# Performance work log

Measured on AMD Instinct MI355X. Metric: run time of the kernel, lower is better.

The kernel has to match this reference:

```python
import jax, jax.numpy as jnp
import numpy as np

EPS = 1e-5
DOWNSAMPLE = 0.5


def setup_inputs() -> dict:
    key = jax.random.key(0)
    k1, k2, k3 = jax.random.split(key, 3)
    B, C, H, W = 32, 256, 128, 128
    x = jax.random.normal(k1, (B, C, H, W), dtype=jnp.float32)
    # 1x1 conv: weight [3, C], bias [3]
    conv_w = jax.random.normal(k2, (3, C), dtype=jnp.float32) / np.sqrt(C).astype(np.float32)
    conv_b = jax.random.normal(k3, (3,), dtype=jnp.float32) * 0.01
    return {"x": x, "conv_w": conv_w, "conv_b": conv_b}


def reference(x, conv_w, conv_b):
    B, C, H, W = x.shape
    dh = int(round(H * DOWNSAMPLE))
    dw = int(round(W * DOWNSAMPLE))

    # 1x1 conv producing 3 channels: 2 offset + 1 attention logit
    oa = jnp.einsum('bchw,oc->bohw', x, conv_w) + conv_b[None, :, None, None]
    offset = oa[:, :2]                      # [B,2,H,W]
    attention = jnp.exp(oa[:, 2:3])         # [B,1,H,W]

    # normalized destination coordinates = base grid + offset, clamped
    gy = jnp.broadcast_to((jnp.arange(H, dtype=x.dtype) / H)[:, None], (H, W))
    gx = jnp.broadcast_to((jnp.arange(W, dtype=x.dtype) / W)[None, :], (H, W))
    base = jnp.stack([gy, gx])              # [2,H,W]
    dest = jnp.clip(base[None] + offset, 0.0, 1.0 - EPS)
    dy = jnp.floor(dest[:, 0] * dh)
    dx = jnp.floor(dest[:, 1] * dw)
    cell = (dy * dw + dx).astype(jnp.int32)  # [B,H,W] spatial cell index

    # full flat destination index over (batch, channel, cell)
    b_off = jnp.arange(B, dtype=jnp.int32)[:, None, None, None] * (C * dh * dw)
    c_off = jnp.arange(C, dtype=jnp.int32)[None, :, None, None] * (dh * dw)
    destination = cell[:, None] + b_off + c_off  # [B,C,H,W]

    # scatter-add attention-weighted features
    xw = (x * attention).reshape(-1)
    feat = jax.ops.segment_sum(xw, destination.reshape(-1), num_segments=B * C * dh * dw)

    # scatter-add attention per (batch, cell) for normalization
    a_idx = cell + jnp.arange(B, dtype=jnp.int32)[:, None, None] * (dh * dw)
    att_sum = jax.ops.segment_sum(attention.reshape(-1), a_idx.reshape(-1), num_segments=B * dh * dw) + EPS

    out = feat.reshape(B, C, dh, dw) / att_sum.reshape(B, 1, dh, dw)
    return (out, offset, destination)
```

## Files before the change

kernel.cpp:

```cpp
#include <hip/hip_runtime.h>
#include <math.h>

#define NB 32
#define NC 256
#define NH 128
#define NW 128
#define NDH 64
#define NDW 64
#define NHW (NH * NW)
#define NCELLS (NDH * NDW)
#define OUT0_N (NB * NC * NCELLS)
#define OUT1_BASE OUT0_N
#define OUT1_N (NB * 2 * NHW)
#define OUT2_BASE (OUT1_BASE + OUT1_N)

#define EPSF 1e-5f

typedef unsigned short u16;
typedef unsigned int   u32;

#define WS_CELLS   ((size_t)0)
#define WS_ATTS    (WS_CELLS + (size_t)NB*NHW*2)
#define WS_ECOMB   (WS_ATTS + (size_t)NB*NHW*4)
#define WS_ASUM    (WS_ECOMB + (size_t)NB*NHW*4)

__device__ __forceinline__ u16 f32_to_bf16_rn(float f) {
    const u32 u = __float_as_uint(f);
    return (u16)((u + 0x7FFFu + ((u >> 16) & 1u)) >> 16);
}

__global__ __launch_bounds__(256) void k_cells(
    const float* __restrict__ x, const float* __restrict__ cw,
    const float* __restrict__ cb, float* __restrict__ out,
    u16* __restrict__ cells, float* __restrict__ atts)
{
    __shared__ float cwS[3][NC];
    __shared__ float red[256][13];

    const int t    = threadIdx.x;
    const int blk  = blockIdx.x;
    const int b    = blk >> 8;
    const int tile = blk & 255;
    const int h    = tile >> 1;
    const int w0   = (tile & 1) << 6;
    const int pixbase = h * NW + w0;

    cwS[0][t] = cw[t];
    cwS[1][t] = cw[NC + t];
    cwS[2][t] = cw[2 * NC + t];
    __syncthreads();

    const int ct = t >> 4;
    const int pg = (t & 15) << 2;
    const float* xb = x + (size_t)b * NC * NHW + pixbase + pg;

    float p00 = 0, p01 = 0, p02 = 0;
    float p10 = 0, p11 = 0, p12 = 0;
    float p20 = 0, p21 = 0, p22 = 0;
    float p30 = 0, p31 = 0, p32 = 0;

    #pragma unroll
    for (int i = 0; i < 16; ++i) {
        const int c = (i << 4) + ct;
        const float4 xv = *reinterpret_cast<const float4*>(xb + (size_t)c * NHW);
        const float wc0 = cwS[0][c], wc1 = cwS[1][c], wc2 = cwS[2][c];
        p00 += xv.x * wc0; p01 += xv.x * wc1; p02 += xv.x * wc2;
        p10 += xv.y * wc0; p11 += xv.y * wc1; p12 += xv.y * wc2;
        p20 += xv.z * wc0; p21 += xv.z * wc1; p22 += xv.z * wc2;
        p30 += xv.w * wc0; p31 += xv.w * wc1; p32 += xv.w * wc2;
    }

    red[t][0]  = p00; red[t][1]  = p01; red[t][2]  = p02;
    red[t][3]  = p10; red[t][4]  = p11; red[t][5]  = p12;
    red[t][6]  = p20; red[t][7]  = p21; red[t][8]  = p22;
    red[t][9]  = p30; red[t][10] = p31; red[t][11] = p32;
    __syncthreads();

    if (t < 64) {
        const int px   = t;
        const int row0 = px >> 2;
        const int col  = (px & 3) * 3;
        float s0 = 0, s1 = 0, s2 = 0;
        #pragma unroll
        for (int j = 0; j < 16; ++j) {
            const int r = row0 + (j << 4);
            s0 += red[r][col];
            s1 += red[r][col + 1];
            s2 += red[r][col + 2];
        }
        const float off0 = s0 + cb[0];
        const float off1 = s1 + cb[1];
        const float att  = expf(s2 + cb[2]);

        const float gy = (float)h * (1.0f / NH);
        const float gx = (float)(w0 + px) * (1.0f / NW);
        const float dyf = fminf(fmaxf(gy + off0, 0.0f), 0.99999f);
        const float dxf = fminf(fmaxf(gx + off1, 0.0f), 0.99999f);
        const int dy = (int)floorf(dyf * (float)NDH);
        const int dx = (int)floorf(dxf * (float)NDW);
        const int cell = dy * NDW + dx;

        cells[b * NHW + pixbase + px] = (u16)cell;
        atts [b * NHW + pixbase + px] = att;

        const int o1 = OUT1_BASE + b * 2 * NHW + pixbase + px;
        out[o1]       = off0;
        out[o1 + NHW] = off1;
    }
}

__global__ __launch_bounds__(1024) void k_sort(
    const u16* __restrict__ cells, const float* __restrict__ atts,
    u32* __restrict__ ecomb, float* __restrict__ asum)
{
    __shared__ u32   hist[NCELLS];
    __shared__ float as_[NCELLS];
    __shared__ u32   ts[1024];

    const int t = threadIdx.x;
    const int b = blockIdx.x;
    const u16*   cb_ = cells + b * NHW;
    const float* ab_ = atts + b * NHW;

    #pragma unroll
    for (int j = 0; j < 4; ++j) { hist[t + 1024 * j] = 0u; as_[t + 1024 * j] = 0.f; }
    __syncthreads();

    #pragma unroll
    for (int j = 0; j < 16; ++j) {
        const int p  = t + 1024 * j;
        const int cl = cb_[p];
        atomicAdd(&hist[cl], 1u);
        atomicAdd(&as_[cl], ab_[p]);
    }
    __syncthreads();

    const u32 h0 = hist[4 * t], h1 = hist[4 * t + 1], h2 = hist[4 * t + 2], h3 = hist[4 * t + 3];
    const u32 T  = h0 + h1 + h2 + h3;
    ts[t] = T;
    __syncthreads();
    for (int off = 1; off < 1024; off <<= 1) {
        const u32 v = (t >= off) ? ts[t - off] : 0u;
        __syncthreads();
        ts[t] += v;
        __syncthreads();
    }
    const u32 base = ts[t] - T;
    hist[4 * t]     = base;
    hist[4 * t + 1] = base + h0;
    hist[4 * t + 2] = base + h0 + h1;
    hist[4 * t + 3] = base + h0 + h1 + h2;

    #pragma unroll
    for (int j = 0; j < 4; ++j)
        asum[b * NCELLS + t + 1024 * j] = as_[t + 1024 * j];
    __syncthreads();

    #pragma unroll
    for (int j = 0; j < 16; ++j) {
        const int p  = t + 1024 * j;
        const int cl = cb_[p];
        const u32 pos = atomicAdd(&hist[cl], 1u);
        ecomb[b * NHW + pos] = ((u32)cl << 16) | (u32)p;
    }
}

#define BF16V(E) __uint_as_float((u32)xpl[(E) & 0xFFFFu] << 16)
#define ACCUM(CUR, S, E, V)                                                   \
    {                                                                         \
        const int cl_ = (int)((E) >> 16);                                     \
        if (cl_ != (CUR)) { atomicAdd(&acc[(CUR)], (S)); (S) = 0.f; (CUR) = cl_; } \
        (S) += (V);                                                           \
    }

__global__ __launch_bounds__(256) void k_gdest(
    const float* __restrict__ x, const float* __restrict__ atts,
    const u16* __restrict__ cells, const u32* __restrict__ ecomb,
    const float* __restrict__ asum, float* __restrict__ out)
{
    __shared__ u16   xpl[NHW];
    __shared__ float acc[NCELLS];

    const int t   = threadIdx.x;
    const int blk = blockIdx.x;
    const int b   = blk >> 8;
    const int c   = blk & 255;

    const float4* xp4  = reinterpret_cast<const float4*>(x + (size_t)(b * NC + c) * NHW);
    const float4* at4  = reinterpret_cast<const float4*>(atts + b * NHW);
    float4*       acc4 = reinterpret_cast<float4*>(acc);

    #pragma unroll
    for (int k = 0; k < 16; ++k) {
        const int idx = t + 256 * k;
        const float4 xv = xp4[idx];
        const float4 av = at4[idx];
        const u32 lo = (u32)f32_to_bf16_rn(xv.x * av.x)
                     | ((u32)f32_to_bf16_rn(xv.y * av.y) << 16);
        const u32 hi = (u32)f32_to_bf16_rn(xv.z * av.z)
                     | ((u32)f32_to_bf16_rn(xv.w * av.w) << 16);
        *reinterpret_cast<uint2*>(&xpl[idx * 4]) = make_uint2(lo, hi);
    }
    const float4 z4 = make_float4(0.f, 0.f, 0.f, 0.f);
    #pragma unroll
    for (int k = 0; k < 4; ++k) acc4[t + 256 * k] = z4;

    {
        const uint2* cl2 = reinterpret_cast<const uint2*>(cells + b * NHW);
        float4* dst4 = reinterpret_cast<float4*>(out + OUT2_BASE + (size_t)(b * NC + c) * NHW);
        const int basec = (b * NC + c) * NCELLS;
        #pragma unroll
        for (int k = 0; k < 16; ++k) {
            const int idx = t + 256 * k;
            const uint2 cc = cl2[idx];
            float4 dv;
            dv.x = (float)(basec + (int)(cc.x & 0xFFFFu));
            dv.y = (float)(basec + (int)(cc.x >> 16));
            dv.z = (float)(basec + (int)(cc.y & 0xFFFFu));
            dv.w = (float)(basec + (int)(cc.y >> 16));
            dst4[idx] = dv;
        }
    }
    __syncthreads();

    {
        const u32* el = ecomb + b * NHW + t * 64;
        float s0 = 0.f, s1 = 0.f, s2 = 0.f, s3 = 0.f;
        int   c0 = (int)(el[0]  >> 16);
        int   c1 = (int)(el[16] >> 16);
        int   c2 = (int)(el[32] >> 16);
        int   c3 = (int)(el[48] >> 16);

        #pragma unroll
        for (int ch = 0; ch < 4; ++ch) {
            const uint4 e0 = *reinterpret_cast<const uint4*>(el + ch * 4);
            const uint4 e1 = *reinterpret_cast<const uint4*>(el + 16 + ch * 4);
            const uint4 e2 = *reinterpret_cast<const uint4*>(el + 32 + ch * 4);
            const uint4 e3 = *reinterpret_cast<const uint4*>(el + 48 + ch * 4);
            const float v00 = BF16V(e0.x), v01 = BF16V(e0.y), v02 = BF16V(e0.z), v03 = BF16V(e0.w);
            const float v10 = BF16V(e1.x), v11 = BF16V(e1.y), v12 = BF16V(e1.z), v13 = BF16V(e1.w);
            const float v20 = BF16V(e2.x), v21 = BF16V(e2.y), v22 = BF16V(e2.z), v23 = BF16V(e2.w);
            const float v30 = BF16V(e3.x), v31 = BF16V(e3.y), v32 = BF16V(e3.z), v33 = BF16V(e3.w);
            ACCUM(c0, s0, e0.x, v00); ACCUM(c1, s1, e1.x, v10); ACCUM(c2, s2, e2.x, v20); ACCUM(c3, s3, e3.x, v30);
            ACCUM(c0, s0, e0.y, v01); ACCUM(c1, s1, e1.y, v11); ACCUM(c2, s2, e2.y, v21); ACCUM(c3, s3, e3.y, v31);
            ACCUM(c0, s0, e0.z, v02); ACCUM(c1, s1, e1.z, v12); ACCUM(c2, s2, e2.z, v22); ACCUM(c3, s3, e3.z, v32);
            ACCUM(c0, s0, e0.w, v03); ACCUM(c1, s1, e1.w, v13); ACCUM(c2, s2, e2.w, v23); ACCUM(c3, s3, e3.w, v33);
        }
        atomicAdd(&acc[c0], s0);
        atomicAdd(&acc[c1], s1);
        atomicAdd(&acc[c2], s2);
        atomicAdd(&acc[c3], s3);
    }
    __syncthreads();

    const float4* as4 = reinterpret_cast<const float4*>(asum + b * NCELLS);
    float4* ob4 = reinterpret_cast<float4*>(out + (size_t)(b * NC + c) * NCELLS);
    #pragma unroll
    for (int k = 0; k < 4; ++k) {
        float4 a = acc4[t + 256 * k];
        const float4 sv = as4[t + 256 * k];
        a.x /= (sv.x + EPSF);
        a.y /= (sv.y + EPSF);
        a.z /= (sv.z + EPSF);
        a.w /= (sv.w + EPSF);
        ob4[t + 256 * k] = a;
    }
}

extern "C" void kernel_launch(void* const* d_in, const int* in_sizes, int n_in,
                              void* d_out, int out_size, void* d_ws, size_t ws_size,
                              hipStream_t stream)
{
    (void)in_sizes; (void)n_in; (void)out_size; (void)ws_size;
    const float* x  = (const float*)d_in[0];
    const float* cw = (const float*)d_in[1];
    const float* cb = (const float*)d_in[2];
    float* out = (float*)d_out;
    char*  ws  = (char*)d_ws;

    u16*   cells = (u16*)  (ws + WS_CELLS);
    float* atts  = (float*)(ws + WS_ATTS);
    u32*   ecomb = (u32*)  (ws + WS_ECOMB);
    float* asum  = (float*)(ws + WS_ASUM);

    k_cells<<<dim3(NB * 256), dim3(256),  0, stream>>>(x, cw, cb, out, cells, atts);
    k_sort <<<dim3(NB),       dim3(1024), 0, stream>>>(cells, atts, ecomb, asum);
    k_gdest<<<dim3(NB * NC),  dim3(256),  0, stream>>>(x, atts, cells, ecomb, asum, out);
}
```

Measured before the change: 476.7 us.

## Move destination output into conv kernel and process four channels per gather block

Result: slower. 944.4 us (+98.1%).

```diff
diff --git a/kernel.cpp b/kernel.cpp
--- a/kernel.cpp
+++ b/kernel.cpp
@@ -20,22 +20,23 @@
 typedef unsigned int   u32;
 
 #define WS_CELLS   ((size_t)0)
-#define WS_ATTS    (WS_CELLS + (size_t)NB*NHW*2)
-#define WS_ECOMB   (WS_ATTS + (size_t)NB*NHW*4)
-#define WS_ASUM    (WS_ECOMB + (size_t)NB*NHW*4)
+#define WS_ATTBF   (WS_CELLS + (size_t)NB*NHW*2)
+#define WS_ECOMB   (WS_ATTBF + (size_t)NB*NHW*2)
+#define WS_IASUM   (WS_ECOMB + (size_t)NB*NHW*4)
 
 __device__ __forceinline__ u16 f32_to_bf16_rn(float f) {
     const u32 u = __float_as_uint(f);
     return (u16)((u + 0x7FFFu + ((u >> 16) & 1u)) >> 16);
 }
 
-__global__ __launch_bounds__(256) void k_cells(
+__global__ __launch_bounds__(256) void k_conv(
     const float* __restrict__ x, const float* __restrict__ cw,
     const float* __restrict__ cb, float* __restrict__ out,
-    u16* __restrict__ cells, float* __restrict__ atts)
+    u16* __restrict__ cells, u16* __restrict__ attbf)
 {
     __shared__ float cwS[3][NC];
     __shared__ float red[256][13];
+    __shared__ int   cellv[64];
 
     const int t    = threadIdx.x;
     const int blk  = blockIdx.x;
@@ -100,18 +101,34 @@
         const int dx = (int)floorf(dxf * (float)NDW);
         const int cell = dy * NDW + dx;
 
+        cellv[px] = cell;
         cells[b * NHW + pixbase + px] = (u16)cell;
-        atts [b * NHW + pixbase + px] = att;
+        attbf[b * NHW + pixbase + px] = f32_to_bf16_rn(att);
 
         const int o1 = OUT1_BASE + b * 2 * NHW + pixbase + px;
         out[o1]       = off0;
         out[o1 + NHW] = off1;
     }
+    __syncthreads();
+
+    const int  c0 = cellv[pg], c1 = cellv[pg + 1], c2 = cellv[pg + 2], c3 = cellv[pg + 3];
+    float* __restrict__ dst = out + OUT2_BASE;
+    #pragma unroll
+    for (int i = 0; i < 16; ++i) {
+        const int c = (i << 4) + ct;
+        const int basec = (b * NC + c) * NCELLS;
+        float4 dv;
+        dv.x = (float)(basec + c0);
+        dv.y = (float)(basec + c1);
+        dv.z = (float)(basec + c2);
+        dv.w = (float)(basec + c3);
+        *reinterpret_cast<float4*>(dst + (size_t)(b * NC + c) * NHW + pixbase + pg) = dv;
+    }
 }
 
 __global__ __launch_bounds__(1024) void k_sort(
-    const u16* __restrict__ cells, const float* __restrict__ atts,
-    u32* __restrict__ ecomb, float* __restrict__ asum)
+    const u16* __restrict__ cells, const u16* __restrict__ attbf,
+    u32* __restrict__ ecomb, float* __restrict__ iasum)
 {
     __shared__ u32   hist[NCELLS];
     __shared__ float as_[NCELLS];
@@ -119,8 +136,8 @@
 
     const int t = threadIdx.x;
     const int b = blockIdx.x;
-    const u16*   cb_ = cells + b * NHW;
-    const float* ab_ = atts + b * NHW;
+    const u16* cb_ = cells + b * NHW;
+    const u16* ab_ = attbf + b * NHW;
 
     #pragma unroll
     for (int j = 0; j < 4; ++j) { hist[t + 1024 * j] = 0u; as_[t + 1024 * j] = 0.f; }
@@ -131,7 +148,7 @@
         const int p  = t + 1024 * j;
         const int cl = cb_[p];
         atomicAdd(&hist[cl], 1u);
-        atomicAdd(&as_[cl], ab_[p]);
+        atomicAdd(&as_[cl], __uint_as_float((u32)ab_[p] << 16));
     }
     __syncthreads();
 
@@ -152,8 +169,10 @@
     hist[4 * t + 3] = base + h0 + h1 + h2;
 
     #pragma unroll
-    for (int j = 0; j < 4; ++j)
-        asum[b * NCELLS + t + 1024 * j] = as_[t + 1024 * j];
+    for (int j = 0; j < 4; ++j) {
+        const int i = t + 1024 * j;
+        iasum[b * NCELLS + i] = 1.0f / (as_[i] + EPSF);
+    }
     __syncthreads();
 
     #pragma unroll
@@ -173,97 +192,125 @@
         (S) += (V);                                                           \
     }
 
-__global__ __launch_bounds__(256) void k_gdest(
-    const float* __restrict__ x, const float* __restrict__ atts,
-    const u16* __restrict__ cells, const u32* __restrict__ ecomb,
-    const float* __restrict__ asum, float* __restrict__ out)
+__global__ __launch_bounds__(256, 3) void k_gd(
+    const float* __restrict__ x, const u16* __restrict__ attbf,
+    const u32* __restrict__ ecomb, const float* __restrict__ iasum,
+    float* __restrict__ out)
 {
     __shared__ u16   xpl[NHW];
     __shared__ float acc[NCELLS];
 
     const int t   = threadIdx.x;
     const int blk = blockIdx.x;
-    const int b   = blk >> 8;
-    const int c   = blk & 255;
-
-    const float4* xp4  = reinterpret_cast<const float4*>(x + (size_t)(b * NC + c) * NHW);
-    const float4* at4  = reinterpret_cast<const float4*>(atts + b * NHW);
-    float4*       acc4 = reinterpret_cast<float4*>(acc);
-
+    const int b   = blk >> 6;
+    const int cg  = (blk & 63) << 2;
+
+    const uint2* ab2 = reinterpret_cast<const uint2*>(attbf + (size_t)b * NHW);
+    uint2 ar[16];
+    #pragma unroll
+    for (int k = 0; k < 16; ++k) ar[k] = ab2[t + 256 * k];
+
+    float4 xr[16];
+    {
+        const float4* xp4 = reinterpret_cast<const float4*>(x + (size_t)(b * NC + cg) * NHW);
+        #pragma unroll
+        for (int k = 0; k < 16; ++k) xr[k] = xp4[t + 256 * k];
+    }
+    float4* acc4 = reinterpret_cast<float4*>(acc);
+    const float4 z4 = make_float4(0.f, 0.f, 0.f, 0.f);
+    #pragma unroll
+    for (int k = 0; k < 4; ++k) acc4[t + 256 * k] = z4;
     #pragma unroll
     for (int k = 0; k < 16; ++k) {
         const int idx = t + 256 * k;
-        const float4 xv = xp4[idx];
-        const float4 av = at4[idx];
-        const u32 lo = (u32)f32_to_bf16_rn(xv.x * av.x)
-                     | ((u32)f32_to_bf16_rn(xv.y * av.y) << 16);
-        const u32 hi = (u32)f32_to_bf16_rn(xv.z * av.z)
-                     | ((u32)f32_to_bf16_rn(xv.w * av.w) << 16);
+        const float a0 = __uint_as_float((u32)ar[k].x << 16);
+        const float a1 = __uint_as_float(ar[k].x & 0xFFFF0000u);
+        const float a2 = __uint_as_float((u32)ar[k].y << 16);
+        const float a3 = __uint_as_float(ar[k].y & 0xFFFF0000u);
+        const u32 lo = (u32)f32_to_bf16_rn(xr[k].x * a0)
+                     | ((u32)f32_to_bf16_rn(xr[k].y * a1) << 16);
+        const u32 hi = (u32)f32_to_bf16_rn(xr[k].z * a2)
+                     | ((u32)f32_to_bf16_rn(xr[k].w * a3) << 16);
         *reinterpret_cast<uint2*>(&xpl[idx * 4]) = make_uint2(lo, hi);
     }
-    const float4 z4 = make_float4(0.f, 0.f, 0.f, 0.f);
-    #pragma unroll
-    for (int k = 0; k < 4; ++k) acc4[t + 256 * k] = z4;
-
-    {
-        const uint2* cl2 = reinterpret_cast<const uint2*>(cells + b * NHW);
-        float4* dst4 = reinterpret_cast<float4*>(out + OUT2_BASE + (size_t)(b * NC + c) * NHW);
-        const int basec = (b * NC + c) * NCELLS;
-        #pragma unroll
-        for (int k = 0; k < 16; ++k) {
-            const int idx = t + 256 * k;
-            const uint2 cc = cl2[idx];
-            float4 dv;
-            dv.x = (float)(basec + (int)(cc.x & 0xFFFFu));
-            dv.y = (float)(basec + (int)(cc.x >> 16));
-            dv.z = (float)(basec + (int)(cc.y & 0xFFFFu));
-            dv.w = (float)(basec + (int)(cc.y >> 16));
-            dst4[idx] = dv;
+    __syncthreads();
+
+    const u32* el = ecomb + b * NHW + t * 64;
+    const float4* ia4 = reinterpret_cast<const float4*>(iasum + b * NCELLS);
+
+    for (int i = 0; i < 4; ++i) {
+        const int c = cg + i;
+
+        if (i < 3) {
+            const float4* xn4 = reinterpret_cast<const float4*>(x + (size_t)(b * NC + c + 1) * NHW);
+            #pragma unroll
+            for (int k = 0; k < 16; ++k) xr[k] = xn4[t + 256 * k];
         }
-    }
-    __syncthreads();
-
-    {
-        const u32* el = ecomb + b * NHW + t * 64;
-        float s0 = 0.f, s1 = 0.f, s2 = 0.f, s3 = 0.f;
-        int   c0 = (int)(el[0]  >> 16);
-        int   c1 = (int)(el[16] >> 16);
-        int   c2 = (int)(el[32] >> 16);
-        int   c3 = (int)(el[48] >> 16);
-
-        #pragma unroll
-        for (int ch = 0; ch < 4; ++ch) {
-            const uint4 e0 = *reinterpret_cast<const uint4*>(el + ch * 4);
-            const uint4 e1 = *reinterpret_cast<const uint4*>(el + 16 + ch * 4);
-            const uint4 e2 = *reinterpret_cast<const uint4*>(el + 32 + ch * 4);
-            const uint4 e3 = *reinterpret_cast<const uint4*>(el + 48 + ch * 4);
-            const float v00 = BF16V(e0.x), v01 = BF16V(e0.y), v02 = BF16V(e0.z), v03 = BF16V(e0.w);
-            const float v10 = BF16V(e1.x), v11 = BF16V(e1.y), v12 = BF16V(e1.z), v13 = BF16V(e1.w);
-            const float v20 = BF16V(e2.x), v21 = BF16V(e2.y), v22 = BF16V(e2.z), v23 = BF16V(e2.w);
-            const float v30 = BF16V(e3.x), v31 = BF16V(e3.y), v32 = BF16V(e3.z), v33 = BF16V(e3.w);
-            ACCUM(c0, s0, e0.x, v00); ACCUM(c1, s1, e1.x, v10); ACCUM(c2, s2, e2.x, v20); ACCUM(c3, s3, e3.x, v30);
-            ACCUM(c0, s0, e0.y, v01); ACCUM(c1, s1, e1.y, v11); ACCUM(c2, s2, e2.y, v21); ACCUM(c3, s3, e3.y, v31);
-            ACCUM(c0, s0, e0.z, v02); ACCUM(c1, s1, e1.z, v12); ACCUM(c2, s2, e2.z, v22); ACCUM(c3, s3, e3.z, v32);
-            ACCUM(c0, s0, e0.w, v03); ACCUM(c1, s1, e1.w, v13); ACCUM(c2, s2, e2.w, v23); ACCUM(c3, s3, e3.w, v33);
+
+        {
+            float s0 = 0.f, s1 = 0.f, s2 = 0.f, s3 = 0.f;
+            int   c0 = (int)(el[0]  >> 16);
+            int   c1 = (int)(el[16] >> 16);
+            int   c2 = (int)(el[32] >> 16);
+            int   c3 = (int)(el[48] >> 16);
+            #pragma unroll
+            for (int ch = 0; ch < 4; ++ch) {
+                const uint4 e0 = *reinterpret_cast<const uint4*>(el + ch * 4);
+                const uint4 e1 = *reinterpret_cast<const uint4*>(el + 16 + ch * 4);
+                const uint4 e2 = *reinterpret_cast<const uint4*>(el + 32 + ch * 4);
+                const uint4 e3 = *reinterpret_cast<const uint4*>(el + 48 + ch * 4);
+                const float v00 = BF16V(e0.x), v01 = BF16V(e0.y), v02 = BF16V(e0.z), v03 = BF16V(e0.w);
+                const float v10 = BF16V(e1.x), v11 = BF16V(e1.y), v12 = BF16V(e1.z), v13 = BF16V(e1.w);
+                const float v20 = BF16V(e2.x), v21 = BF16V(e2.y), v22 = BF16V(e2.z), v23 = BF16V(e2.w);
+                const float v30 = BF16V(e3.x), v31 = BF16V(e3.y), v32 = BF16V(e3.z), v33 = BF16V(e3.w);
+                ACCUM(c0, s0, e0.x, v00); ACCUM(c1, s1, e1.x, v10); ACCUM(c2, s2, e2.x, v20); ACCUM(c3, s3, e3.x, v30);
+                ACCUM(c0, s0, e0.y, v01); ACCUM(c1, s1, e1.y, v11); ACCUM(c2, s2, e2.y, v21); ACCUM(c3, s3, e3.y, v31);
+                ACCUM(c0, s0, e0.z, v02); ACCUM(c1, s1, e1.z, v12); ACCUM(c2, s2, e2.z, v22); ACCUM(c3, s3, e3.z, v32);
+                ACCUM(c0, s0, e0.w, v03); ACCUM(c1, s1, e1.w, v13); ACCUM(c2, s2, e2.w, v23); ACCUM(c3, s3, e3.w, v33);
+            }
+            atomicAdd(&acc[c0], s0);
+            atomicAdd(&acc[c1], s1);
+            atomicAdd(&acc[c2], s2);
+            atomicAdd(&acc[c3], s3);
         }
-        atomicAdd(&acc[c0], s0);
-        atomicAdd(&acc[c1], s1);
-        atomicAdd(&acc[c2], s2);
-        atomicAdd(&acc[c3], s3);
-    }
-    __syncthreads();
-
-    const float4* as4 = reinterpret_cast<const float4*>(asum + b * NCELLS);
-    float4* ob4 = reinterpret_cast<float4*>(out + (size_t)(b * NC + c) * NCELLS);
-    #pragma unroll
-    for (int k = 0; k < 4; ++k) {
-        float4 a = acc4[t + 256 * k];
-        const float4 sv = as4[t + 256 * k];
-        a.x /= (sv.x + EPSF);
-        a.y /= (sv.y + EPSF);
-        a.z /= (sv.z + EPSF);
-        a.w /= (sv.w + EPSF);
-        ob4[t + 256 * k] = a;
+        __syncthreads();
+
+        float4 a0 = acc4[t];
+        float4 a1 = acc4[t + 256];
+        float4 a2 = acc4[t + 512];
+        float4 a3 = acc4[t + 768];
+
+        if (i < 3) {
+            #pragma unroll
+            for (int k = 0; k < 16; ++k) {
+                const int idx = t + 256 * k;
+                const float b0 = __uint_as_float((u32)ar[k].x << 16);
+                const float b1 = __uint_as_float(ar[k].x & 0xFFFF0000u);
+                const float b2 = __uint_as_float((u32)ar[k].y << 16);
+                const float b3 = __uint_as_float(ar[k].y & 0xFFFF0000u);
+                const u32 lo = (u32)f32_to_bf16_rn(xr[k].x * b0)
+                             | ((u32)f32_to_bf16_rn(xr[k].y * b1) << 16);
+                const u32 hi = (u32)f32_to_bf16_rn(xr[k].z * b2)
+                             | ((u32)f32_to_bf16_rn(xr[k].w * b3) << 16);
+                *reinterpret_cast<uint2*>(&xpl[idx * 4]) = make_uint2(lo, hi);
+            }
+        }
+        acc4[t]       = z4;
+        acc4[t + 256] = z4;
+        acc4[t + 512] = z4;
+        acc4[t + 768] = z4;
+
+        float4* ob4 = reinterpret_cast<float4*>(out + (size_t)(b * NC + c) * NCELLS);
+        const float4 i0 = ia4[t], i1 = ia4[t + 256], i2 = ia4[t + 512], i3 = ia4[t + 768];
+        a0.x *= i0.x; a0.y *= i0.y; a0.z *= i0.z; a0.w *= i0.w;
+        a1.x *= i1.x; a1.y *= i1.y; a1.z *= i1.z; a1.w *= i1.w;
+        a2.x *= i2.x; a2.y *= i2.y; a2.z *= i2.z; a2.w *= i2.w;
+        a3.x *= i3.x; a3.y *= i3.y; a3.z *= i3.z; a3.w *= i3.w;
+        ob4[t]       = a0;
+        ob4[t + 256] = a1;
+        ob4[t + 512] = a2;
+        ob4[t + 768] = a3;
+        __syncthreads();
     }
 }
 
@@ -279,11 +326,11 @@
     char*  ws  = (char*)d_ws;
 
     u16*   cells = (u16*)  (ws + WS_CELLS);
-    float* atts  = (float*)(ws + WS_ATTS);
+    u16*   attbf = (u16*)  (ws + WS_ATTBF);
     u32*   ecomb = (u32*)  (ws + WS_ECOMB);
-    float* asum  = (float*)(ws + WS_ASUM);
-
-    k_cells<<<dim3(NB * 256), dim3(256),  0, stream>>>(x, cw, cb, out, cells, atts);
-    k_sort <<<dim3(NB),       dim3(1024), 0, stream>>>(cells, atts, ecomb, asum);
-    k_gdest<<<dim3(NB * NC),  dim3(256),  0, stream>>>(x, atts, cells, ecomb, asum, out);
-}
+    float* iasum = (float*)(ws + WS_IASUM);
+
+    k_conv<<<dim3(NB * 256), dim3(256),  0, stream>>>(x, cw, cb, out, cells, attbf);
+    k_sort<<<dim3(NB),       dim3(1024), 0, stream>>>(cells, attbf, ecomb, iasum);
+    k_gd  <<<dim3(NB * 64),  dim3(256),  0, stream>>>(x, attbf, ecomb, iasum, out);
+}
```
